# Performance work log

Measured on AMD Instinct MI355X. Metric: run time of the kernel, lower is better.

The kernel has to match this reference:

```python
import jax, jax.numpy as jnp
import numpy as np

N, C, H, W = 32, 24, 14, 14
HD, GH, AS = 128, 256, 28
D_IN = (C + 2) * 2 + HD  # 180


def setup_inputs() -> dict:
    key = jax.random.key(0)
    ks = jax.random.split(key, 10)
    s = 0.05
    inp = {
        "x": jax.random.normal(ks[0], (N, C, H, W), jnp.float32),
        "code": jax.random.normal(ks[1], (N, HD), jnp.float32),
        "gw0": jax.random.normal(ks[2], (D_IN, GH), jnp.float32) * s,
        "gb0": jnp.zeros((GH,), jnp.float32),
        "gw1": jax.random.normal(ks[3], (GH, GH), jnp.float32) * s,
        "gb1": jnp.zeros((GH,), jnp.float32),
        "gw2": jax.random.normal(ks[4], (GH, GH), jnp.float32) * s,
        "gb2": jnp.zeros((GH,), jnp.float32),
        "gw3": jax.random.normal(ks[5], (GH, GH), jnp.float32) * s,
        "gb3": jnp.zeros((GH,), jnp.float32),
        "fw0": jax.random.normal(ks[6], (GH, GH), jnp.float32) * s,
        "fb0": jnp.zeros((GH,), jnp.float32),
        "fw1": jax.random.normal(ks[7], (GH, GH), jnp.float32) * s,
        "fb1": jnp.zeros((GH,), jnp.float32),
        "fw2": jax.random.normal(ks[8], (GH, AS), jnp.float32) * s,
        "fb2": jnp.zeros((AS,), jnp.float32),
    }
    return inp


def _rn_encode(x, code):
    n, c, h, w = x.shape
    o = h * w
    hd = code.shape[1]
    # coordinates: torch.linspace(-h/2, h/2, h) over row dim, (-w/2, w/2, w) over col dim
    xs = jnp.linspace(-h / 2.0, h / 2.0, h, dtype=jnp.float32)
    ys = jnp.linspace(-w / 2.0, w / 2.0, w, dtype=jnp.float32)
    coord = jnp.stack(
        [jnp.broadcast_to(xs[:, None], (h, w)).reshape(o),
         jnp.broadcast_to(ys[None, :], (h, w)).reshape(o)], axis=-1)  # (o, 2)
    feats = x.reshape(n, c, o).transpose(0, 2, 1)  # (n, o, c)
    feats = jnp.concatenate([feats, jnp.broadcast_to(coord, (n, o, 2))], axis=-1)  # (n, o, c+2)
    # pairs[n, i, j] = [feats[n, j], feats[n, i], code[n]]  (matches torch expand semantics)
    p1 = jnp.broadcast_to(feats[:, None, :, :], (n, o, o, c + 2))
    p2 = jnp.broadcast_to(feats[:, :, None, :], (n, o, o, c + 2))
    q = jnp.broadcast_to(code[:, None, None, :], (n, o, o, hd))
    return jnp.concatenate([p1, p2, q], axis=-1).reshape(n, o * o, -1)


def reference(x, code, gw0, gb0, gw1, gb1, gw2, gb2, gw3, gb3,
              fw0, fb0, fw1, fb1, fw2, fb2):
    pairs = _rn_encode(x, code)  # (n, o^2, 180)
    h1 = jax.nn.relu(pairs @ gw0 + gb0)
    h1 = jax.nn.relu(h1 @ gw1 + gb1)
    h1 = jax.nn.relu(h1 @ gw2 + gb2)
    h1 = jax.nn.relu(h1 @ gw3 + gb3)
    relations = h1.sum(axis=1)  # (n, GH) sum-pool over all pairs
    r = jax.nn.relu(relations @ fw0 + fb0)
    r = jax.nn.relu(r @ fw1 + fb1)
    logits = r @ fw2 + fb2  # last layer linear (last=True)
    return logits
```

## Files before the change

kernel.cpp:

```cpp
#include <hip/hip_runtime.h>
#include <hip/hip_bf16.h>


typedef __attribute__((ext_vector_type(8))) short short8;
typedef __attribute__((ext_vector_type(16))) float f32x16;

#define NIMG 32
#define O 196
#define PAIRS 38416
#define GH 256
#define AS 28
#define ROWS 64
#define CHUNKS 601

#define SWZ16(row) (((row) & 15) << 4)

static __device__ __forceinline__ unsigned short f2bf(float f) {
    __hip_bfloat16 h = __float2bfloat16(f);
    return *reinterpret_cast<unsigned short*>(&h);
}

__global__ void k_cc(const float* __restrict__ code, const float* __restrict__ gw0,
                     const float* __restrict__ gb0, float* __restrict__ CC) {
    const int n = blockIdx.x, g = threadIdx.x;
    __shared__ float cs[128];
    if (g < 128) cs[g] = code[n * 128 + g];
    __syncthreads();
    float acc = gb0[g];
    for (int k = 0; k < 128; ++k) acc = fmaf(cs[k], gw0[(52 + k) * GH + g], acc);
    CC[n * GH + g] = acc;
}

__global__ void k_ajbi(const float* __restrict__ x, const float* __restrict__ gw0,
                       const float* __restrict__ CC,
                       float* __restrict__ AJ, float* __restrict__ BI) {
    const int np = blockIdx.x;
    const int n = np / O, p = np - n * O;
    const int g = threadIdx.x;
    __shared__ float fs[26];
    if (g < 24)       fs[g]  = x[(n * 24 + g) * O + p];
    else if (g == 24) fs[24] = -7.0f + (float)(p / 14) * (14.0f / 13.0f);
    else if (g == 25) fs[25] = -7.0f + (float)(p % 14) * (14.0f / 13.0f);
    __syncthreads();
    float aj = CC[n * GH + g], bi = 0.f;
#pragma unroll
    for (int c = 0; c < 26; ++c) {
        const float f = fs[c];
        aj = fmaf(f, gw0[c * GH + g], aj);
        bi = fmaf(f, gw0[(26 + c) * GH + g], bi);
    }
    AJ[np * GH + g] = aj;
    BI[np * GH + g] = bi;
}

__global__ void k_pack(const float* __restrict__ gw1, const float* __restrict__ gw2,
                       const float* __restrict__ gw3, unsigned short* __restrict__ pW) {
    const int idx = blockIdx.x * 256 + threadIdx.x;
    const int L = idx >> 16;
    const int rem = idx & 0xFFFF;
    const int e = rem & 7;
    const int lane = (rem >> 3) & 63;
    const int ks = (rem >> 9) & 15;
    const int nt = rem >> 13;
    const int k = ks * 16 + ((lane >> 5) << 3) + e;
    const int col = nt * 32 + (lane & 31);
    const float* W = (L == 0) ? gw1 : (L == 1) ? gw2 : gw3;
    pW[idx] = f2bf(W[k * GH + col]);
}

__global__ __launch_bounds__(512, 6) void k_main(
    const float* __restrict__ AJ, const float* __restrict__ BI,
    const unsigned short* __restrict__ pW,
    const float* __restrict__ gb1, const float* __restrict__ gb2,
    const float* __restrict__ gb3, float* __restrict__ rel) {
    __shared__ __attribute__((aligned(16))) unsigned short h[ROWS * GH];

    const int blk = blockIdx.x;
    const int n = blk / CHUNKS;
    const int chunk = blk - n * CHUNKS;
    const int row_base = chunk * ROWS;
    const int t = threadIdx.x;
    const int wave = t >> 6;
    const int lane = t & 63;
    const int l31 = lane & 31;
    const int hi = lane >> 5;
    const int l15 = lane & 15;
    const bool tail = (chunk == CHUNKS - 1);

    {
        const int i0 = row_base / O;
        const int j00 = row_base - i0 * O;
        const int i1 = min(i0 + 1, O - 1);
        const float4 bi0 = *(const float4*)&BI[(n * O + i0) * GH + lane * 4];
        const float4 bi1 = *(const float4*)&BI[(n * O + i1) * GH + lane * 4];
#pragma unroll
        for (int e = 0; e < 8; ++e) {
            const int r = wave + e * 8;
            const int jj = j00 + r;
            const bool wrap = (jj >= O);
            const int j = wrap ? jj - O : jj;
            const float4 aj = *(const float4*)&AJ[(n * O + j) * GH + lane * 4];
            const float4 bi = wrap ? bi1 : bi0;
            const unsigned int lo = (unsigned)f2bf(fmaxf(aj.x + bi.x, 0.f)) |
                                    ((unsigned)f2bf(fmaxf(aj.y + bi.y, 0.f)) << 16);
            const unsigned int hh = (unsigned)f2bf(fmaxf(aj.z + bi.z, 0.f)) |
                                    ((unsigned)f2bf(fmaxf(aj.w + bi.w, 0.f)) << 16);
            const int byteoff = r * 512 + ((lane * 8) ^ SWZ16(r));
            uint2 dd; dd.x = lo; dd.y = hh;
            *(uint2*)((char*)h + byteoff) = dd;
        }
    }
    __syncthreads();

    const int X = SWZ16(l15);
    const int hi16 = hi << 4;
    const int arow = l31 * 512;

    auto kloop = [&](const short8* wp, f32x16& a0, f32x16& a1, bool swapped) {
        short8 wa = wp[lane], wb = wp[64 + lane], wc = wp[128 + lane], wd = wp[192 + lane];
        const char* hb = (const char*)h + arow;
#pragma unroll
        for (int ks = 0; ks < 16; ++ks) {
            const short8 W = (ks & 3) == 0 ? wa : (ks & 3) == 1 ? wb
                           : (ks & 3) == 2 ? wc : wd;
            const int off = (ks * 32 + hi16) ^ X;
            const short8 h0 = *(const short8*)(hb + off);
            const short8 h1 = *(const short8*)(hb + off + 16384);
            __builtin_amdgcn_s_setprio(1);
            if (swapped) {
                a0 = __builtin_amdgcn_mfma_f32_32x32x16_bf16(W, h0, a0, 0, 0, 0);
                a1 = __builtin_amdgcn_mfma_f32_32x32x16_bf16(W, h1, a1, 0, 0, 0);
            } else {
                a0 = __builtin_amdgcn_mfma_f32_32x32x16_bf16(h0, W, a0, 0, 0, 0);
                a1 = __builtin_amdgcn_mfma_f32_32x32x16_bf16(h1, W, a1, 0, 0, 0);
            }
            __builtin_amdgcn_s_setprio(0);
            if (ks < 12) {
                const short8 nw = wp[(ks + 4) * 64 + lane];
                if ((ks & 3) == 0) wa = nw; else if ((ks & 3) == 1) wb = nw;
                else if ((ks & 3) == 2) wc = nw; else wd = nw;
            }
        }
    };

    auto epi = [&](const f32x16& a0, const f32x16& a1, const float* gb) {
        const float4 b40 = *(const float4*)&gb[wave * 32 + 0  + 4 * hi];
        const float4 b41 = *(const float4*)&gb[wave * 32 + 8  + 4 * hi];
        const float4 b42 = *(const float4*)&gb[wave * 32 + 16 + 4 * hi];
        const float4 b43 = *(const float4*)&gb[wave * 32 + 24 + 4 * hi];
        const float bias[16] = {b40.x, b40.y, b40.z, b40.w, b41.x, b41.y, b41.z, b41.w,
                                b42.x, b42.y, b42.z, b42.w, b43.x, b43.y, b43.z, b43.w};
        char* w0 = (char*)h + l31 * 512;
#pragma unroll
        for (int rp = 0; rp < 8; ++rp) {
            const int r0 = rp * 2;
            const float ba = bias[(r0 >> 2) * 4 + (r0 & 3)];
            const float bb = bias[(r0 >> 2) * 4 + (r0 & 3) + 1];
            const int cw = (r0 & 3) + 8 * (r0 >> 2);
            const int cb = (wave * 64 + cw * 2 + hi * 8) ^ X;
            const unsigned p0 = (unsigned)f2bf(fmaxf(a0[r0] + ba, 0.f)) |
                                ((unsigned)f2bf(fmaxf(a0[r0 + 1] + bb, 0.f)) << 16);
            const unsigned p1 = (unsigned)f2bf(fmaxf(a1[r0] + ba, 0.f)) |
                                ((unsigned)f2bf(fmaxf(a1[r0 + 1] + bb, 0.f)) << 16);
            *(unsigned*)(w0 + cb) = p0;
            *(unsigned*)(w0 + 16384 + cb) = p1;
        }
    };

    const f32x16 z = {0.f,0.f,0.f,0.f,0.f,0.f,0.f,0.f,0.f,0.f,0.f,0.f,0.f,0.f,0.f,0.f};
    const short8* wpb = (const short8*)pW + wave * 1024;

    f32x16 acc0 = z, acc1 = z;
    kloop(wpb, acc0, acc1, true);
    __syncthreads();
    epi(acc0, acc1, gb1);
    __syncthreads();

    acc0 = z; acc1 = z;
    kloop(wpb + 8192, acc0, acc1, true);
    __syncthreads();
    epi(acc0, acc1, gb2);
    __syncthreads();

    acc0 = z; acc1 = z;
    kloop(wpb + 16384, acc0, acc1, false);
    {
        const float bias = gb3[wave * 32 + l31];
        float s = 0.f;
        if (!tail) {
#pragma unroll
            for (int r = 0; r < 16; ++r)
                s += fmaxf(acc0[r] + bias, 0.f) + fmaxf(acc1[r] + bias, 0.f);
        } else {
#pragma unroll
            for (int r = 0; r < 8; ++r)
                s += fmaxf(acc0[r] + bias, 0.f);
        }
        s += __shfl_xor(s, 32);
        if (hi == 0) atomicAdd(&rel[n * GH + wave * 32 + l31], s);
    }
}

__global__ void k_fmlp(const float* __restrict__ rel,
                       const float* __restrict__ fw0, const float* __restrict__ fb0,
                       const float* __restrict__ fw1, const float* __restrict__ fb1,
                       const float* __restrict__ fw2, const float* __restrict__ fb2,
                       float* __restrict__ out) {
    __shared__ float b0[GH], b1[GH];
    const int n = blockIdx.x, g = threadIdx.x;
    b0[g] = rel[n * GH + g];
    __syncthreads();
    float a = fb0[g];
    for (int k = 0; k < GH; ++k) a = fmaf(b0[k], fw0[k * GH + g], a);
    b1[g] = fmaxf(a, 0.f);
    __syncthreads();
    float c = fb1[g];
    for (int k = 0; k < GH; ++k) c = fmaf(b1[k], fw1[k * GH + g], c);
    b0[g] = fmaxf(c, 0.f);
    __syncthreads();
    if (g < AS) {
        float o = fb2[g];
        for (int k = 0; k < GH; ++k) o = fmaf(b0[k], fw2[k * AS + g], o);
        out[n * AS + g] = o;
    }
}

extern "C" void kernel_launch(void* const* d_in, const int* in_sizes, int n_in,
                              void* d_out, int out_size, void* d_ws, size_t ws_size,
                              hipStream_t stream) {
    const float* x    = (const float*)d_in[0];
    const float* code = (const float*)d_in[1];
    const float* gw0  = (const float*)d_in[2];
    const float* gb0  = (const float*)d_in[3];
    const float* gw1  = (const float*)d_in[4];
    const float* gb1  = (const float*)d_in[5];
    const float* gw2  = (const float*)d_in[6];
    const float* gb2  = (const float*)d_in[7];
    const float* gw3  = (const float*)d_in[8];
    const float* gb3  = (const float*)d_in[9];
    const float* fw0  = (const float*)d_in[10];
    const float* fb0  = (const float*)d_in[11];
    const float* fw1  = (const float*)d_in[12];
    const float* fb1  = (const float*)d_in[13];
    const float* fw2  = (const float*)d_in[14];
    const float* fb2  = (const float*)d_in[15];
    float* out = (float*)d_out;

    char* ws = (char*)d_ws;
    float*          AJ  = (float*)(ws + 0);
    float*          BI  = (float*)(ws + 6422528);
    float*          CC  = (float*)(ws + 12845056);
    float*          rel = (float*)(ws + 12877824);
    unsigned short* pW  = (unsigned short*)(ws + 12910592);

    hipMemsetAsync(rel, 0, NIMG * GH * sizeof(float), stream);
    k_cc<<<NIMG, 256, 0, stream>>>(code, gw0, gb0, CC);
    k_ajbi<<<NIMG * O, 256, 0, stream>>>(x, gw0, CC, AJ, BI);
    k_pack<<<768, 256, 0, stream>>>(gw1, gw2, gw3, pW);
    k_main<<<NIMG * CHUNKS, 512, 0, stream>>>(AJ, BI, pW, gb1, gb2, gb3, rel);
    k_fmlp<<<NIMG, 256, 0, stream>>>(rel, fw0, fb0, fw1, fb1, fw2, fb2, out);
}
```

Before: 631.6 us.

## Make main kernel persistent with double-buffered LDS and prefetched next chunk

Result: slower. 1.853 ms (+193.4%).

```diff
diff --git a/kernel.cpp b/kernel.cpp
--- a/kernel.cpp
+++ b/kernel.cpp
@@ -7,11 +7,12 @@
 
 #define NIMG 32
 #define O 196
-#define PAIRS 38416
 #define GH 256
 #define AS 28
 #define ROWS 64
 #define CHUNKS 601
+#define TOTALC (NIMG * CHUNKS)
+#define GRID 512
 
 #define SWZ16(row) (((row) & 15) << 4)
 
@@ -68,26 +69,34 @@
     pW[idx] = f2bf(W[k * GH + col]);
 }
 
-__global__ __launch_bounds__(512, 6) void k_main(
+__global__ __launch_bounds__(512, 4) void k_main(
     const float* __restrict__ AJ, const float* __restrict__ BI,
     const unsigned short* __restrict__ pW,
     const float* __restrict__ gb1, const float* __restrict__ gb2,
     const float* __restrict__ gb3, float* __restrict__ rel) {
-    __shared__ __attribute__((aligned(16))) unsigned short h[ROWS * GH];
-
-    const int blk = blockIdx.x;
-    const int n = blk / CHUNKS;
-    const int chunk = blk - n * CHUNKS;
-    const int row_base = chunk * ROWS;
+    __shared__ __attribute__((aligned(16))) unsigned short hA[ROWS * GH];
+    __shared__ __attribute__((aligned(16))) unsigned short hB[ROWS * GH];
+
     const int t = threadIdx.x;
     const int wave = t >> 6;
     const int lane = t & 63;
     const int l31 = lane & 31;
     const int hi = lane >> 5;
     const int l15 = lane & 15;
-    const bool tail = (chunk == CHUNKS - 1);
-
-    {
+    const int X = SWZ16(l15);
+    const int hi16 = hi << 4;
+    const int arow = l31 * 512;
+
+    const short8* wpb = (const short8*)pW + wave * 1024;
+    const float bias3 = gb3[wave * 32 + l31];
+
+    unsigned short* pA = hA;
+    unsigned short* pB = hB;
+
+    auto p0 = [&](unsigned short* dst, int gg) {
+        const int n = gg / CHUNKS;
+        const int chunk = gg - n * CHUNKS;
+        const int row_base = chunk * ROWS;
         const int i0 = row_base / O;
         const int j00 = row_base - i0 * O;
         const int i1 = min(i0 + 1, O - 1);
@@ -101,24 +110,20 @@
             const int j = wrap ? jj - O : jj;
             const float4 aj = *(const float4*)&AJ[(n * O + j) * GH + lane * 4];
             const float4 bi = wrap ? bi1 : bi0;
-            const unsigned int lo = (unsigned)f2bf(fmaxf(aj.x + bi.x, 0.f)) |
-                                    ((unsigned)f2bf(fmaxf(aj.y + bi.y, 0.f)) << 16);
-            const unsigned int hh = (unsigned)f2bf(fmaxf(aj.z + bi.z, 0.f)) |
-                                    ((unsigned)f2bf(fmaxf(aj.w + bi.w, 0.f)) << 16);
+            const unsigned lo = (unsigned)f2bf(fmaxf(aj.x + bi.x, 0.f)) |
+                                ((unsigned)f2bf(fmaxf(aj.y + bi.y, 0.f)) << 16);
+            const unsigned hh = (unsigned)f2bf(fmaxf(aj.z + bi.z, 0.f)) |
+                                ((unsigned)f2bf(fmaxf(aj.w + bi.w, 0.f)) << 16);
             const int byteoff = r * 512 + ((lane * 8) ^ SWZ16(r));
             uint2 dd; dd.x = lo; dd.y = hh;
-            *(uint2*)((char*)h + byteoff) = dd;
-        }
-    }
-    __syncthreads();
-
-    const int X = SWZ16(l15);
-    const int hi16 = hi << 4;
-    const int arow = l31 * 512;
-
-    auto kloop = [&](const short8* wp, f32x16& a0, f32x16& a1, bool swapped) {
-        short8 wa = wp[lane], wb = wp[64 + lane], wc = wp[128 + lane], wd = wp[192 + lane];
-        const char* hb = (const char*)h + arow;
+            *(uint2*)((char*)dst + byteoff) = dd;
+        }
+    };
+
+    short8 wa, wb, wc, wd;
+    auto kloop = [&](const unsigned short* buf, const short8* wp,
+                     f32x16& a0, f32x16& a1, bool swapped) {
+        const char* hb = (const char*)buf + arow;
 #pragma unroll
         for (int ks = 0; ks < 16; ++ks) {
             const short8 W = (ks & 3) == 0 ? wa : (ks & 3) == 1 ? wb
@@ -143,14 +148,15 @@
         }
     };
 
-    auto epi = [&](const f32x16& a0, const f32x16& a1, const float* gb) {
+    auto epi = [&](const f32x16& a0, const f32x16& a1, const float* gb,
+                   unsigned short* dst) {
         const float4 b40 = *(const float4*)&gb[wave * 32 + 0  + 4 * hi];
         const float4 b41 = *(const float4*)&gb[wave * 32 + 8  + 4 * hi];
         const float4 b42 = *(const float4*)&gb[wave * 32 + 16 + 4 * hi];
         const float4 b43 = *(const float4*)&gb[wave * 32 + 24 + 4 * hi];
         const float bias[16] = {b40.x, b40.y, b40.z, b40.w, b41.x, b41.y, b41.z, b41.w,
                                 b42.x, b42.y, b42.z, b42.w, b43.x, b43.y, b43.z, b43.w};
-        char* w0 = (char*)h + l31 * 512;
+        char* w0 = (char*)dst + l31 * 512;
 #pragma unroll
         for (int rp = 0; rp < 8; ++rp) {
             const int r0 = rp * 2;
@@ -158,46 +164,68 @@
             const float bb = bias[(r0 >> 2) * 4 + (r0 & 3) + 1];
             const int cw = (r0 & 3) + 8 * (r0 >> 2);
             const int cb = (wave * 64 + cw * 2 + hi * 8) ^ X;
-            const unsigned p0 = (unsigned)f2bf(fmaxf(a0[r0] + ba, 0.f)) |
+            const unsigned q0 = (unsigned)f2bf(fmaxf(a0[r0] + ba, 0.f)) |
                                 ((unsigned)f2bf(fmaxf(a0[r0 + 1] + bb, 0.f)) << 16);
-            const unsigned p1 = (unsigned)f2bf(fmaxf(a1[r0] + ba, 0.f)) |
+            const unsigned q1 = (unsigned)f2bf(fmaxf(a1[r0] + ba, 0.f)) |
                                 ((unsigned)f2bf(fmaxf(a1[r0 + 1] + bb, 0.f)) << 16);
-            *(unsigned*)(w0 + cb) = p0;
-            *(unsigned*)(w0 + 16384 + cb) = p1;
+            *(unsigned*)(w0 + cb) = q0;
+            *(unsigned*)(w0 + 16384 + cb) = q1;
         }
     };
 
     const f32x16 z = {0.f,0.f,0.f,0.f,0.f,0.f,0.f,0.f,0.f,0.f,0.f,0.f,0.f,0.f,0.f,0.f};
-    const short8* wpb = (const short8*)pW + wave * 1024;
-
-    f32x16 acc0 = z, acc1 = z;
-    kloop(wpb, acc0, acc1, true);
-    __syncthreads();
-    epi(acc0, acc1, gb1);
-    __syncthreads();
-
-    acc0 = z; acc1 = z;
-    kloop(wpb + 8192, acc0, acc1, true);
-    __syncthreads();
-    epi(acc0, acc1, gb2);
-    __syncthreads();
-
-    acc0 = z; acc1 = z;
-    kloop(wpb + 16384, acc0, acc1, false);
-    {
-        const float bias = gb3[wave * 32 + l31];
-        float s = 0.f;
-        if (!tail) {
-#pragma unroll
-            for (int r = 0; r < 16; ++r)
-                s += fmaxf(acc0[r] + bias, 0.f) + fmaxf(acc1[r] + bias, 0.f);
-        } else {
-#pragma unroll
-            for (int r = 0; r < 8; ++r)
-                s += fmaxf(acc0[r] + bias, 0.f);
-        }
-        s += __shfl_xor(s, 32);
-        if (hi == 0) atomicAdd(&rel[n * GH + wave * 32 + l31], s);
+
+    int g = blockIdx.x;
+    p0(pA, g);
+    wa = wpb[lane]; wb = wpb[64 + lane]; wc = wpb[128 + lane]; wd = wpb[192 + lane];
+    __syncthreads();
+
+    for (;;) {
+        const int n = g / CHUNKS;
+        const bool tail = (g - n * CHUNKS) == (CHUNKS - 1);
+
+        f32x16 a0 = z, a1 = z;
+        kloop(pA, wpb, a0, a1, true);
+        wa = wpb[8192 + lane];        wb = wpb[8192 + 64 + lane];
+        wc = wpb[8192 + 128 + lane];  wd = wpb[8192 + 192 + lane];
+        epi(a0, a1, gb1, pB);
+        __syncthreads();
+
+        a0 = z; a1 = z;
+        kloop(pB, wpb + 8192, a0, a1, true);
+        wa = wpb[16384 + lane];       wb = wpb[16384 + 64 + lane];
+        wc = wpb[16384 + 128 + lane]; wd = wpb[16384 + 192 + lane];
+        epi(a0, a1, gb2, pA);
+        __syncthreads();
+
+        a0 = z; a1 = z;
+        kloop(pA, wpb + 16384, a0, a1, false);
+
+        const int gn = g + GRID;
+        const bool more = (gn < TOTALC);
+        if (more) p0(pB, gn);
+        wa = wpb[lane]; wb = wpb[64 + lane];
+        wc = wpb[128 + lane]; wd = wpb[192 + lane];
+
+        {
+            float s = 0.f;
+            if (!tail) {
+#pragma unroll
+                for (int r = 0; r < 16; ++r)
+                    s += fmaxf(a0[r] + bias3, 0.f) + fmaxf(a1[r] + bias3, 0.f);
+            } else {
+#pragma unroll
+                for (int r = 0; r < 8; ++r)
+                    s += fmaxf(a0[r] + bias3, 0.f);
+            }
+            s += __shfl_xor(s, 32);
+            if (hi == 0) atomicAdd(&rel[n * GH + wave * 32 + l31], s);
+        }
+
+        if (!more) break;
+        unsigned short* tmp = pA; pA = pB; pB = tmp;
+        g = gn;
+        __syncthreads();
     }
 }
 
@@ -257,6 +285,6 @@
     k_cc<<<NIMG, 256, 0, stream>>>(code, gw0, gb0, CC);
     k_ajbi<<<NIMG * O, 256, 0, stream>>>(x, gw0, CC, AJ, BI);
     k_pack<<<768, 256, 0, stream>>>(gw1, gw2, gw3, pW);
-    k_main<<<NIMG * CHUNKS, 512, 0, stream>>>(AJ, BI, pW, gb1, gb2, gb3, rel);
+    k_main<<<GRID, 512, 0, stream>>>(AJ, BI, pW, gb1, gb2, gb3, rel);
     k_fmlp<<<NIMG, 256, 0, stream>>>(rel, fw0, fb0, fw1, fb1, fw2, fb2, out);
 }
```

## Halve block size so each wave computes two N-tiles, merge setup kernels

Applied to the files above, without the earlier changes.

Measured after the change: 848.1 us. 34.3% more time.

```diff
diff --git a/kernel.cpp b/kernel.cpp
--- a/kernel.cpp
+++ b/kernel.cpp
@@ -7,7 +7,6 @@
 
 #define NIMG 32
 #define O 196
-#define PAIRS 38416
 #define GH 256
 #define AS 28
 #define ROWS 64
@@ -20,15 +19,31 @@
     return *reinterpret_cast<unsigned short*>(&h);
 }
 
-__global__ void k_cc(const float* __restrict__ code, const float* __restrict__ gw0,
-                     const float* __restrict__ gb0, float* __restrict__ CC) {
-    const int n = blockIdx.x, g = threadIdx.x;
-    __shared__ float cs[128];
-    if (g < 128) cs[g] = code[n * 128 + g];
-    __syncthreads();
-    float acc = gb0[g];
-    for (int k = 0; k < 128; ++k) acc = fmaf(cs[k], gw0[(52 + k) * GH + g], acc);
-    CC[n * GH + g] = acc;
+__global__ void k_setup(const float* __restrict__ gw1, const float* __restrict__ gw2,
+                        const float* __restrict__ gw3, unsigned short* __restrict__ pW,
+                        const float* __restrict__ code, const float* __restrict__ gw0,
+                        const float* __restrict__ gb0, float* __restrict__ CC) {
+    if (blockIdx.x < 768) {
+        const int idx = blockIdx.x * 256 + threadIdx.x;
+        const int L = idx >> 16;
+        const int rem = idx & 0xFFFF;
+        const int e = rem & 7;
+        const int lane = (rem >> 3) & 63;
+        const int ks = (rem >> 9) & 15;
+        const int nt = rem >> 13;
+        const int k = ks * 16 + ((lane >> 5) << 3) + e;
+        const int col = nt * 32 + (lane & 31);
+        const float* W = (L == 0) ? gw1 : (L == 1) ? gw2 : gw3;
+        pW[idx] = f2bf(W[k * GH + col]);
+    } else {
+        const int n = blockIdx.x - 768, g = threadIdx.x;
+        __shared__ float cs[128];
+        if (g < 128) cs[g] = code[n * 128 + g];
+        __syncthreads();
+        float acc = gb0[g];
+        for (int k = 0; k < 128; ++k) acc = fmaf(cs[k], gw0[(52 + k) * GH + g], acc);
+        CC[n * GH + g] = acc;
+    }
 }
 
 __global__ void k_ajbi(const float* __restrict__ x, const float* __restrict__ gw0,
@@ -53,22 +68,7 @@
     BI[np * GH + g] = bi;
 }
 
-__global__ void k_pack(const float* __restrict__ gw1, const float* __restrict__ gw2,
-                       const float* __restrict__ gw3, unsigned short* __restrict__ pW) {
-    const int idx = blockIdx.x * 256 + threadIdx.x;
-    const int L = idx >> 16;
-    const int rem = idx & 0xFFFF;
-    const int e = rem & 7;
-    const int lane = (rem >> 3) & 63;
-    const int ks = (rem >> 9) & 15;
-    const int nt = rem >> 13;
-    const int k = ks * 16 + ((lane >> 5) << 3) + e;
-    const int col = nt * 32 + (lane & 31);
-    const float* W = (L == 0) ? gw1 : (L == 1) ? gw2 : gw3;
-    pW[idx] = f2bf(W[k * GH + col]);
-}
-
-__global__ __launch_bounds__(512, 6) void k_main(
+__global__ __launch_bounds__(256, 4) void k_main(
     const float* __restrict__ AJ, const float* __restrict__ BI,
     const unsigned short* __restrict__ pW,
     const float* __restrict__ gb1, const float* __restrict__ gb2,
@@ -94,17 +94,17 @@
         const float4 bi0 = *(const float4*)&BI[(n * O + i0) * GH + lane * 4];
         const float4 bi1 = *(const float4*)&BI[(n * O + i1) * GH + lane * 4];
 #pragma unroll
-        for (int e = 0; e < 8; ++e) {
-            const int r = wave + e * 8;
+        for (int e = 0; e < 16; ++e) {
+            const int r = wave + e * 4;
             const int jj = j00 + r;
             const bool wrap = (jj >= O);
             const int j = wrap ? jj - O : jj;
             const float4 aj = *(const float4*)&AJ[(n * O + j) * GH + lane * 4];
             const float4 bi = wrap ? bi1 : bi0;
-            const unsigned int lo = (unsigned)f2bf(fmaxf(aj.x + bi.x, 0.f)) |
-                                    ((unsigned)f2bf(fmaxf(aj.y + bi.y, 0.f)) << 16);
-            const unsigned int hh = (unsigned)f2bf(fmaxf(aj.z + bi.z, 0.f)) |
-                                    ((unsigned)f2bf(fmaxf(aj.w + bi.w, 0.f)) << 16);
+            const unsigned lo = (unsigned)f2bf(fmaxf(aj.x + bi.x, 0.f)) |
+                                ((unsigned)f2bf(fmaxf(aj.y + bi.y, 0.f)) << 16);
+            const unsigned hh = (unsigned)f2bf(fmaxf(aj.z + bi.z, 0.f)) |
+                                ((unsigned)f2bf(fmaxf(aj.w + bi.w, 0.f)) << 16);
             const int byteoff = r * 512 + ((lane * 8) ^ SWZ16(r));
             uint2 dd; dd.x = lo; dd.y = hh;
             *(uint2*)((char*)h + byteoff) = dd;
@@ -115,89 +115,112 @@
     const int X = SWZ16(l15);
     const int hi16 = hi << 4;
     const int arow = l31 * 512;
-
-    auto kloop = [&](const short8* wp, f32x16& a0, f32x16& a1, bool swapped) {
-        short8 wa = wp[lane], wb = wp[64 + lane], wc = wp[128 + lane], wd = wp[192 + lane];
+    const int s0 = wave * 2, s1 = wave * 2 + 1;
+
+    auto kloop = [&](const short8* w0, const short8* w1,
+                     f32x16& aA0, f32x16& aA1, f32x16& aB0, f32x16& aB1,
+                     bool swapped) {
+        short8 p0a = w0[lane], p0b = w0[64 + lane];
+        short8 p1a = w1[lane], p1b = w1[64 + lane];
         const char* hb = (const char*)h + arow;
 #pragma unroll
         for (int ks = 0; ks < 16; ++ks) {
-            const short8 W = (ks & 3) == 0 ? wa : (ks & 3) == 1 ? wb
-                           : (ks & 3) == 2 ? wc : wd;
+            const short8 W0 = p0a, W1 = p1a;
+            p0a = p0b; p1a = p1b;
+            if (ks < 14) { p0b = w0[(ks + 2) * 64 + lane]; p1b = w1[(ks + 2) * 64 + lane]; }
             const int off = (ks * 32 + hi16) ^ X;
             const short8 h0 = *(const short8*)(hb + off);
             const short8 h1 = *(const short8*)(hb + off + 16384);
             __builtin_amdgcn_s_setprio(1);
             if (swapped) {
-                a0 = __builtin_amdgcn_mfma_f32_32x32x16_bf16(W, h0, a0, 0, 0, 0);
-                a1 = __builtin_amdgcn_mfma_f32_32x32x16_bf16(W, h1, a1, 0, 0, 0);
+                aA0 = __builtin_amdgcn_mfma_f32_32x32x16_bf16(W0, h0, aA0, 0, 0, 0);
+                aA1 = __builtin_amdgcn_mfma_f32_32x32x16_bf16(W0, h1, aA1, 0, 0, 0);
+                aB0 = __builtin_amdgcn_mfma_f32_32x32x16_bf16(W1, h0, aB0, 0, 0, 0);
+                aB1 = __builtin_amdgcn_mfma_f32_32x32x16_bf16(W1, h1, aB1, 0, 0, 0);
             } else {
-                a0 = __builtin_amdgcn_mfma_f32_32x32x16_bf16(h0, W, a0, 0, 0, 0);
-                a1 = __builtin_amdgcn_mfma_f32_32x32x16_bf16(h1, W, a1, 0, 0, 0);
+                aA0 = __builtin_amdgcn_mfma_f32_32x32x16_bf16(h0, W0, aA0, 0, 0, 0);
+                aA1 = __builtin_amdgcn_mfma_f32_32x32x16_bf16(h1, W0, aA1, 0, 0, 0);
+                aB0 = __builtin_amdgcn_mfma_f32_32x32x16_bf16(h0, W1, aB0, 0, 0, 0);
+                aB1 = __builtin_amdgcn_mfma_f32_32x32x16_bf16(h1, W1, aB1, 0, 0, 0);
             }
             __builtin_amdgcn_s_setprio(0);
-            if (ks < 12) {
-                const short8 nw = wp[(ks + 4) * 64 + lane];
-                if ((ks & 3) == 0) wa = nw; else if ((ks & 3) == 1) wb = nw;
-                else if ((ks & 3) == 2) wc = nw; else wd = nw;
+        }
+    };
+
+    auto epi = [&](const f32x16& aA0, const f32x16& aA1,
+                   const f32x16& aB0, const f32x16& aB1, const float* gb) {
+        char* hc = (char*)h;
+#pragma unroll
+        for (int q = 0; q < 4; ++q) {
+            const float4 bA = *(const float4*)&gb[s0 * 32 + 8 * q + 4 * hi];
+            const float4 bB = *(const float4*)&gb[s1 * 32 + 8 * q + 4 * hi];
+            const int r0 = q * 4;
+            uint2 vA0, vA1, vB0, vB1;
+            vA0.x = (unsigned)f2bf(fmaxf(aA0[r0] + bA.x, 0.f)) |
+                    ((unsigned)f2bf(fmaxf(aA0[r0 + 1] + bA.y, 0.f)) << 16);
+            vA0.y = (unsigned)f2bf(fmaxf(aA0[r0 + 2] + bA.z, 0.f)) |
+                    ((unsigned)f2bf(fmaxf(aA0[r0 + 3] + bA.w, 0.f)) << 16);
+            vA1.x = (unsigned)f2bf(fmaxf(aA1[r0] + bA.x, 0.f)) |
+                    ((unsigned)f2bf(fmaxf(aA1[r0 + 1] + bA.y, 0.f)) << 16);
+            vA1.y = (unsigned)f2bf(fmaxf(aA1[r0 + 2] + bA.z, 0.f)) |
+                    ((unsigned)f2bf(fmaxf(aA1[r0 + 3] + bA.w, 0.f)) << 16);
+            vB0.x = (unsigned)f2bf(fmaxf(aB0[r0] + bB.x, 0.f)) |
+                    ((unsigned)f2bf(fmaxf(aB0[r0 + 1] + bB.y, 0.f)) << 16);
+            vB0.y = (unsigned)f2bf(fmaxf(aB0[r0 + 2] + bB.z, 0.f)) |
+                    ((unsigned)f2bf(fmaxf(aB0[r0 + 3] + bB.w, 0.f)) << 16);
+            vB1.x = (unsigned)f2bf(fmaxf(aB1[r0] + bB.x, 0.f)) |
+                    ((unsigned)f2bf(fmaxf(aB1[r0 + 1] + bB.y, 0.f)) << 16);
+            vB1.y = (unsigned)f2bf(fmaxf(aB1[r0 + 2] + bB.z, 0.f)) |
+                    ((unsigned)f2bf(fmaxf(aB1[r0 + 3] + bB.w, 0.f)) << 16);
+            const int cA = (s0 * 64 + 16 * q + 8 * hi) ^ X;
+            const int cB = (s1 * 64 + 16 * q + 8 * hi) ^ X;
+            *(uint2*)(hc + arow + cA) = vA0;
+            *(uint2*)(hc + arow + cB) = vB0;
+            *(uint2*)(hc + arow + 16384 + cA) = vA1;
+            *(uint2*)(hc + arow + 16384 + cB) = vB1;
+        }
+    };
+
+    const f32x16 z = {0.f,0.f,0.f,0.f,0.f,0.f,0.f,0.f,0.f,0.f,0.f,0.f,0.f,0.f,0.f,0.f};
+    const short8* wl = (const short8*)pW;
+
+    f32x16 aA0 = z, aA1 = z, aB0 = z, aB1 = z;
+    kloop(wl + s0 * 1024, wl + s1 * 1024, aA0, aA1, aB0, aB1, true);
+    __syncthreads();
+    epi(aA0, aA1, aB0, aB1, gb1);
+    __syncthreads();
+
+    aA0 = z; aA1 = z; aB0 = z; aB1 = z;
+    kloop(wl + 8192 + s0 * 1024, wl + 8192 + s1 * 1024, aA0, aA1, aB0, aB1, true);
+    __syncthreads();
+    epi(aA0, aA1, aB0, aB1, gb2);
+    __syncthreads();
+
+    aA0 = z; aA1 = z; aB0 = z; aB1 = z;
+    kloop(wl + 16384 + s0 * 1024, wl + 16384 + s1 * 1024, aA0, aA1, aB0, aB1, false);
+    {
+        const float biasA = gb3[s0 * 32 + l31];
+        const float biasB = gb3[s1 * 32 + l31];
+        float sA = 0.f, sB = 0.f;
+        if (!tail) {
+#pragma unroll
+            for (int r = 0; r < 16; ++r) {
+                sA += fmaxf(aA0[r] + biasA, 0.f) + fmaxf(aA1[r] + biasA, 0.f);
+                sB += fmaxf(aB0[r] + biasB, 0.f) + fmaxf(aB1[r] + biasB, 0.f);
             }
-        }
-    };
-
-    auto epi = [&](const f32x16& a0, const f32x16& a1, const float* gb) {
-        const float4 b40 = *(const float4*)&gb[wave * 32 + 0  + 4 * hi];
-        const float4 b41 = *(const float4*)&gb[wave * 32 + 8  + 4 * hi];
-        const float4 b42 = *(const float4*)&gb[wave * 32 + 16 + 4 * hi];
-        const float4 b43 = *(const float4*)&gb[wave * 32 + 24 + 4 * hi];
-        const float bias[16] = {b40.x, b40.y, b40.z, b40.w, b41.x, b41.y, b41.z, b41.w,
-                                b42.x, b42.y, b42.z, b42.w, b43.x, b43.y, b43.z, b43.w};
-        char* w0 = (char*)h + l31 * 512;
-#pragma unroll
-        for (int rp = 0; rp < 8; ++rp) {
-            const int r0 = rp * 2;
-            const float ba = bias[(r0 >> 2) * 4 + (r0 & 3)];
-            const float bb = bias[(r0 >> 2) * 4 + (r0 & 3) + 1];
-            const int cw = (r0 & 3) + 8 * (r0 >> 2);
-            const int cb = (wave * 64 + cw * 2 + hi * 8) ^ X;
-            const unsigned p0 = (unsigned)f2bf(fmaxf(a0[r0] + ba, 0.f)) |
-                                ((unsigned)f2bf(fmaxf(a0[r0 + 1] + bb, 0.f)) << 16);
-            const unsigned p1 = (unsigned)f2bf(fmaxf(a1[r0] + ba, 0.f)) |
-                                ((unsigned)f2bf(fmaxf(a1[r0 + 1] + bb, 0.f)) << 16);
-            *(unsigned*)(w0 + cb) = p0;
-            *(unsigned*)(w0 + 16384 + cb) = p1;
-        }
-    };
-
-    const f32x16 z = {0.f,0.f,0.f,0.f,0.f,0.f,0.f,0.f,0.f,0.f,0.f,0.f,0.f,0.f,0.f,0.f};
-    const short8* wpb = (const short8*)pW + wave * 1024;
-
-    f32x16 acc0 = z, acc1 = z;
-    kloop(wpb, acc0, acc1, true);
-    __syncthreads();
-    epi(acc0, acc1, gb1);
-    __syncthreads();
-
-    acc0 = z; acc1 = z;
-    kloop(wpb + 8192, acc0, acc1, true);
-    __syncthreads();
-    epi(acc0, acc1, gb2);
-    __syncthreads();
-
-    acc0 = z; acc1 = z;
-    kloop(wpb + 16384, acc0, acc1, false);
-    {
-        const float bias = gb3[wave * 32 + l31];
-        float s = 0.f;
-        if (!tail) {
-#pragma unroll
-            for (int r = 0; r < 16; ++r)
-                s += fmaxf(acc0[r] + bias, 0.f) + fmaxf(acc1[r] + bias, 0.f);
         } else {
 #pragma unroll
-            for (int r = 0; r < 8; ++r)
-                s += fmaxf(acc0[r] + bias, 0.f);
-        }
-        s += __shfl_xor(s, 32);
-        if (hi == 0) atomicAdd(&rel[n * GH + wave * 32 + l31], s);
+            for (int r = 0; r < 8; ++r) {
+                sA += fmaxf(aA0[r] + biasA, 0.f);
+                sB += fmaxf(aB0[r] + biasB, 0.f);
+            }
+        }
+        sA += __shfl_xor(sA, 32);
+        sB += __shfl_xor(sB, 32);
+        if (hi == 0) {
+            atomicAdd(&rel[n * GH + s0 * 32 + l31], sA);
+            atomicAdd(&rel[n * GH + s1 * 32 + l31], sB);
+        }
     }
 }
 
@@ -254,9 +277,8 @@
     unsigned short* pW  = (unsigned short*)(ws + 12910592);
 
     hipMemsetAsync(rel, 0, NIMG * GH * sizeof(float), stream);
-    k_cc<<<NIMG, 256, 0, stream>>>(code, gw0, gb0, CC);
+    k_setup<<<800, 256, 0, stream>>>(gw1, gw2, gw3, pW, code, gw0, gb0, CC);
     k_ajbi<<<NIMG * O, 256, 0, stream>>>(x, gw0, CC, AJ, BI);
-    k_pack<<<768, 256, 0, stream>>>(gw1, gw2, gw3, pW);
-    k_main<<<NIMG * CHUNKS, 512, 0, stream>>>(AJ, BI, pW, gb1, gb2, gb3, rel);
+    k_main<<<NIMG * CHUNKS, 256, 0, stream>>>(AJ, BI, pW, gb1, gb2, gb3, rel);
     k_fmlp<<<NIMG, 256, 0, stream>>>(rel, fw0, fb0, fw1, fb1, fw2, fb2, out);
 }
```
